# Kernel tuning notes

Hardware: AMD Instinct MI355X
Metric: run time of the kernel (lower is better)

## Reference

```python
import jax, jax.numpy as jnp
import numpy as np
import math

BLOCK = 8
N_COEFF = BLOCK * BLOCK  # 64
N_SAMPLE = 250
SEED = 0  # args.seed

# zigzag order: flat index m*8+n from the hardcoded loc table
ZIGZAG = jnp.array([
    0, 1, 8, 16, 9, 2, 3, 10, 17, 24, 32, 25, 18, 11, 4, 5,
    12, 19, 26, 33, 40, 48, 41, 34, 27, 20, 13, 6, 7, 14, 21, 28,
    35, 42, 49, 56, 57, 50, 43, 36, 29, 22, 15, 23, 30, 37, 44, 51,
    58, 59, 52, 45, 38, 31, 39, 46, 53, 60, 61, 54, 47, 55, 62, 63
], dtype=jnp.int32)


def dct_matrix():
    Q = np.zeros((BLOCK, BLOCK), dtype=np.float32)
    Q[0, :] = math.sqrt(1.0 / BLOCK)
    for i in range(1, BLOCK):
        for j in range(BLOCK):
            Q[i, j] = math.sqrt(2.0 / BLOCK) * math.cos((2 * j + 1) * math.pi * i / (2.0 * BLOCK))
    return jnp.asarray(Q)


def setup_inputs() -> dict:
    key = jax.random.key(0)
    x = jax.random.uniform(key, (64, 3, 512, 512), dtype=jnp.float32)
    return {"x": x}


def reference(x):
    Q = dct_matrix()
    # rgb -> ycbcr, luminance channel only (module discards Cb/Cr)
    x255 = x * 255.0
    y = (0.299 * x255[:, 0] + 0.587 * x255[:, 1] + 0.114 * x255[:, 2]) / 255.0  # [B,H,W]
    B, H, W = y.shape
    a, b = H // BLOCK, W // BLOCK
    # split into 8x8 blocks: [B, a, b, 8, 8]
    blocks = y.reshape(B, a, BLOCK, b, BLOCK).transpose(0, 1, 3, 2, 4)
    # per-block 2D DCT: Q @ block @ Q^T, batched as one einsum
    dct = jnp.einsum('ij,nabjk,lk->nabil', Q, blocks, Q)  # [B,a,b,8,8]
    image_dct_result = dct.transpose(0, 1, 3, 2, 4).reshape(B, 1, H, W)
    # zigzag gather over flattened block coefficients -> [B, 64, a*b]
    dist = dct.reshape(B, a * b, N_COEFF)[:, :, ZIGZAG].transpose(0, 2, 1)
    # per (sample, coefficient) random permutation sampling of 250 blocks
    keys = jax.random.split(jax.random.key(SEED), B * N_COEFF)
    idx = jax.vmap(lambda k: jax.random.permutation(k, a * b)[:N_SAMPLE])(keys)
    idx = idx.reshape(B, N_COEFF, N_SAMPLE)
    dct_coeff_sample = jnp.take_along_axis(dist, idx, axis=2)  # [B,64,250]
    return image_dct_result, dct_coeff_sample
```

## Files before the change

kernel.cpp:

```cpp
#include <hip/hip_runtime.h>
#include <hip/hip_bf16.h>
#include <cstdint>


#define BATCH 64
#define HW 512
#define NBLK 4096
#define NSAMPLE 250
#define IMG_ELEMS (HW * HW)

#define A0 0.35355339059327373f
#define A1 0.49039264020161522f
#define A2 0.46193976625564337f
#define A3 0.41573480615127262f
#define A4 0.35355339059327379f
#define A5 0.27778511650980111f
#define A6 0.19134171618254492f
#define A7 0.09754516100806412f

__constant__ float Qc[8][8] = {
    { A0,  A0,  A0,  A0,  A0,  A0,  A0,  A0},
    { A1,  A3,  A5,  A7, -A7, -A5, -A3, -A1},
    { A2,  A6, -A6, -A2, -A2, -A6,  A6,  A2},
    { A3, -A7, -A1, -A5,  A5,  A1,  A7, -A3},
    { A4, -A4, -A4,  A4,  A4, -A4, -A4,  A4},
    { A5, -A1,  A7,  A3, -A3, -A7,  A1, -A5},
    { A6, -A2,  A2, -A6, -A6,  A2, -A2,  A6},
    { A7, -A5,  A3, -A1,  A1, -A3,  A5, -A7},
};

__constant__ int ZIGZAG[64] = {
    0, 1, 8, 16, 9, 2, 3, 10, 17, 24, 32, 25, 18, 11, 4, 5,
    12, 19, 26, 33, 40, 48, 41, 34, 27, 20, 13, 6, 7, 14, 21, 28,
    35, 42, 49, 56, 57, 50, 43, 36, 29, 22, 15, 23, 30, 37, 44, 51,
    58, 59, 52, 45, 38, 31, 39, 46, 53, 60, 61, 54, 47, 55, 62, 63
};

__device__ __forceinline__ uint32_t rotl32(uint32_t v, int d) {
    return (v << d) | (v >> (32 - d));
}

__device__ __forceinline__ void tf2x32(uint32_t k0, uint32_t k1,
                                       uint32_t x0, uint32_t x1,
                                       uint32_t& o0, uint32_t& o1) {
    uint32_t ks0 = k0, ks1 = k1, ks2 = k0 ^ k1 ^ 0x1BD11BDAu;
    x0 += ks0; x1 += ks1;
#define TF_R(r) { x0 += x1; x1 = rotl32(x1, r); x1 ^= x0; }
    TF_R(13) TF_R(15) TF_R(26) TF_R(6)
    x0 += ks1; x1 += ks2 + 1u;
    TF_R(17) TF_R(29) TF_R(16) TF_R(24)
    x0 += ks2; x1 += ks0 + 2u;
    TF_R(13) TF_R(15) TF_R(26) TF_R(6)
    x0 += ks0; x1 += ks1 + 3u;
    TF_R(17) TF_R(29) TF_R(16) TF_R(24)
    x0 += ks1; x1 += ks2 + 4u;
    TF_R(13) TF_R(15) TF_R(26) TF_R(6)
    x0 += ks2; x1 += ks0 + 5u;
#undef TF_R
    o0 = x0; o1 = x1;
}

__device__ __forceinline__ void build4096(
    uint32_t s0, uint32_t s1,
    uint32_t* __restrict__ pack32, uint32_t* __restrict__ hist,
    int tid, int w, int lane, uint32_t* __restrict__ wsum) {

    __syncthreads();
    ((uint4*)hist)[tid] = make_uint4(0u, 0u, 0u, 0u);
    ((uint4*)hist)[tid + 512] = make_uint4(0u, 0u, 0u, 0u);
    uint32_t keys[8];
#pragma unroll
    for (int e = 0; e < 8; ++e) {
        uint32_t o0, o1;
        tf2x32(s0, s1, 0u, (uint32_t)(tid + e * 512), o0, o1);
        keys[e] = o0 ^ o1;
    }
    __syncthreads();

    uint32_t ord[8];
#pragma unroll
    for (int e = 0; e < 8; ++e)
        ord[e] = atomicAdd(&hist[keys[e] >> 20], 1u);
    __syncthreads();

    uint4 va = ((const uint4*)hist)[tid * 2];
    uint4 vb = ((const uint4*)hist)[tid * 2 + 1];
    uint32_t ssum = va.x + va.y + va.z + va.w + vb.x + vb.y + vb.z + vb.w;
    uint32_t sc = ssum;
#pragma unroll
    for (int off = 1; off < 64; off <<= 1) {
        uint32_t t = __shfl_up(sc, off);
        if (lane >= off) sc += t;
    }
    if (lane == 63) wsum[w] = sc;
    __syncthreads();
    uint32_t ex = sc - ssum;
    for (int ww = 0; ww < w; ++ww) ex += wsum[ww];
    uint32_t p1 = ex + va.x, p2 = p1 + va.y, p3 = p2 + va.z, p4 = p3 + va.w;
    uint32_t p5 = p4 + vb.x, p6 = p5 + vb.y, p7 = p6 + vb.z, p8 = p7 + vb.w;
    ((uint4*)hist)[tid * 2] = make_uint4(p1, p2, p3, p4);
    ((uint4*)hist)[tid * 2 + 1] = make_uint4(p5, p6, p7, p8);
    __syncthreads();

#pragma unroll
    for (int e = 0; e < 8; ++e) {
        uint32_t bkt = keys[e] >> 20;
        uint32_t start = bkt ? hist[bkt - 1] : 0u;
        pack32[start + ord[e]] =
            ((keys[e] & 0xFFFFFu) << 12) | (uint32_t)(tid + e * 512);
    }
}

__device__ __forceinline__ uint32_t select4096(
    const uint32_t* __restrict__ hist, const uint32_t* __restrict__ pack32,
    uint32_t s) {
    uint32_t lo = 0, hi = 4095;
#pragma unroll
    for (int it = 0; it < 12; ++it) {
        uint32_t mid = (lo + hi) >> 1;
        if (hist[mid] > s) hi = mid; else lo = mid + 1;
    }
    uint32_t b = lo;
    uint32_t start = b ? hist[b - 1] : 0u;
    uint32_t L = hist[b] - start;
    uint32_t c = pack32[start];
    if (L > 1) {
        uint32_t k = s - start;
        for (uint32_t cand = 0; cand < L; ++cand) {
            uint32_t cc = pack32[start + cand];
            uint32_t cnt = 0;
            for (uint32_t o = 0; o < L; ++o)
                cnt += (pack32[start + o] < cc) ? 1u : 0u;
            if (cnt == k) { c = cc; break; }
        }
    }
    return c & 0xFFFu;
}

__global__ __launch_bounds__(512, 8) void fused_kernel(
    const float* __restrict__ x, float* __restrict__ out,
    uint32_t* __restrict__ ws) {
    __shared__ __align__(16) uint8_t smem[33280];
    __shared__ uint32_t wsum[8];

    const int tid = threadIdx.x;
    const int grp = (int)blockIdx.x / 9;
    const int rem = (int)blockIdx.x % 9;

    if (rem == 8) {
        int g = grp * 512 + tid;
        int b = g >> 12;
        int rr = g & 4095;
        int ai = rr >> 6, bi = rr & 63;
        int row0 = ai * 8, col0 = bi * 8;
        size_t ib = (size_t)b * 3 * IMG_ELEMS;
        size_t ob = (size_t)b * IMG_ELEMS;

#pragma unroll 1
        for (int p = 0; p < 4; ++p) {
            float acc[2][8];
#pragma unroll
            for (int j = 0; j < 8; ++j) { acc[0][j] = 0.0f; acc[1][j] = 0.0f; }

#pragma unroll 1
            for (int k = 0; k < 8; ++k) {
                size_t off = ib + (size_t)(row0 + k) * HW + col0;
                float y[8];
                {
                    float4 r0 = *(const float4*)(x + off);
                    float4 g0 = *(const float4*)(x + off + IMG_ELEMS);
                    float4 b0 = *(const float4*)(x + off + 2 * IMG_ELEMS);
                    y[0] = (0.299f * (r0.x * 255.0f) + 0.587f * (g0.x * 255.0f) +
                            0.114f * (b0.x * 255.0f)) / 255.0f;
                    y[1] = (0.299f * (r0.y * 255.0f) + 0.587f * (g0.y * 255.0f) +
                            0.114f * (b0.y * 255.0f)) / 255.0f;
                    y[2] = (0.299f * (r0.z * 255.0f) + 0.587f * (g0.z * 255.0f) +
                            0.114f * (b0.z * 255.0f)) / 255.0f;
                    y[3] = (0.299f * (r0.w * 255.0f) + 0.587f * (g0.w * 255.0f) +
                            0.114f * (b0.w * 255.0f)) / 255.0f;
                }
                {
                    float4 r1 = *(const float4*)(x + off + 4);
                    float4 g1 = *(const float4*)(x + off + IMG_ELEMS + 4);
                    float4 b1 = *(const float4*)(x + off + 2 * IMG_ELEMS + 4);
                    y[4] = (0.299f * (r1.x * 255.0f) + 0.587f * (g1.x * 255.0f) +
                            0.114f * (b1.x * 255.0f)) / 255.0f;
                    y[5] = (0.299f * (r1.y * 255.0f) + 0.587f * (g1.y * 255.0f) +
                            0.114f * (b1.y * 255.0f)) / 255.0f;
                    y[6] = (0.299f * (r1.z * 255.0f) + 0.587f * (g1.z * 255.0f) +
                            0.114f * (b1.z * 255.0f)) / 255.0f;
                    y[7] = (0.299f * (r1.w * 255.0f) + 0.587f * (g1.w * 255.0f) +
                            0.114f * (b1.w * 255.0f)) / 255.0f;
                }
                float q0 = Qc[p * 2][k], q1 = Qc[p * 2 + 1][k];
#pragma unroll
                for (int j = 0; j < 8; ++j) {
                    acc[0][j] += q0 * y[j];
                    acc[1][j] += q1 * y[j];
                }
            }

#pragma unroll
            for (int i2 = 0; i2 < 2; ++i2) {
                float d[8];
#pragma unroll
                for (int j = 0; j < 8; ++j) {
                    float s = 0.0f;
#pragma unroll
                    for (int k = 0; k < 8; ++k) s += acc[i2][k] * Qc[j][k];
                    d[j] = s;
                }
                float4* o = (float4*)(out + ob +
                                      (size_t)(row0 + p * 2 + i2) * HW + col0);
                o[0] = make_float4(d[0], d[1], d[2], d[3]);
                o[1] = make_float4(d[4], d[5], d[6], d[7]);
            }
        }
    } else {
        uint32_t* pack32 = (uint32_t*)smem;
        uint32_t* hist = (uint32_t*)(smem + 16384);
        uint16_t* jsel = (uint16_t*)(smem + 32768);

        const int w = tid >> 6;
        const int lane = tid & 63;
        const int gb = grp * 8 + rem;

        uint32_t k0, k1, n0, n1, sA0, sA1, sB0, sB1;
        tf2x32(0u, 0u, 0u, (uint32_t)gb, k0, k1);
        tf2x32(k0, k1, 0u, 0u, n0, n1);
        tf2x32(k0, k1, 0u, 1u, sA0, sA1);
        tf2x32(n0, n1, 0u, 1u, sB0, sB1);

        build4096(sB0, sB1, pack32, hist, tid, w, lane, wsum);
        __syncthreads();
        if (tid < NSAMPLE)
            jsel[tid] = (uint16_t)select4096(hist, pack32, (uint32_t)tid);

        build4096(sA0, sA1, pack32, hist, tid, w, lane, wsum);
        __syncthreads();

        int b = gb >> 6, c = gb & 63;
        int z = ZIGZAG[c];
        int i0z = z >> 3, j0z = z & 7;
        if (tid < NSAMPLE) {
            uint32_t i = select4096(hist, pack32, (uint32_t)jsel[tid]);
            int ai = (int)i >> 6, bi = (int)i & 63;
            ws[(size_t)gb * 256 + tid] =
                (uint32_t)((size_t)b * IMG_ELEMS +
                           (size_t)(ai * 8 + i0z) * HW + (bi * 8 + j0z));
        }
    }
}

__global__ __launch_bounds__(256) void gather_kernel(
    const float* __restrict__ img, const uint32_t* __restrict__ ws,
    float* __restrict__ out2) {
    const int gb = blockIdx.x;
    const int s = threadIdx.x;
    if (s < NSAMPLE)
        out2[(size_t)gb * NSAMPLE + s] = img[ws[(size_t)gb * 256 + s]];
}

extern "C" void kernel_launch(void* const* d_in, const int* in_sizes, int n_in,
                              void* d_out, int out_size, void* d_ws, size_t ws_size,
                              hipStream_t stream) {
    const float* x = (const float*)d_in[0];
    float* out = (float*)d_out;
    uint32_t* ws = (uint32_t*)d_ws;
    fused_kernel<<<512 * 9, 512, 0, stream>>>(x, out, ws);
    gather_kernel<<<BATCH * 64, 256, 0, stream>>>(
        out, ws, out + (size_t)BATCH * IMG_ELEMS);
}
```

Before: 411.4 us.

## Merge DCT work into every permutation block with LDS-staged luma rows

Each of the 4096 blocks now computes the DCT for one 8-pixel-high image row strip before doing its own permutation-sampling work. This replaces the separate DCT-only blocks that ran alongside the sampling blocks. Luma values are staged in shared memory so that the loads and the row transform are spread across threads. The aim is to balance memory-bound and compute-bound work inside each block and to cut the grid size. The risk is that shared memory is reused for pack32 with no visible barrier after the DCT reads, which could race.

```diff
diff --git a/kernel.cpp b/kernel.cpp
--- a/kernel.cpp
+++ b/kernel.cpp
@@ -144,86 +144,81 @@
     __shared__ uint32_t wsum[8];
 
     const int tid = threadIdx.x;
-    const int grp = (int)blockIdx.x / 9;
-    const int rem = (int)blockIdx.x % 9;
-
-    if (rem == 8) {
-        int g = grp * 512 + tid;
-        int b = g >> 12;
-        int rr = g & 4095;
-        int ai = rr >> 6, bi = rr & 63;
-        int row0 = ai * 8, col0 = bi * 8;
-        size_t ib = (size_t)b * 3 * IMG_ELEMS;
-        size_t ob = (size_t)b * IMG_ELEMS;
-
-#pragma unroll 1
-        for (int p = 0; p < 4; ++p) {
-            float acc[2][8];
-#pragma unroll
-            for (int j = 0; j < 8; ++j) { acc[0][j] = 0.0f; acc[1][j] = 0.0f; }
-
-#pragma unroll 1
+    const int gb = blockIdx.x;
+
+    {
+        float* ylds = (float*)smem;
+        const int b = gb >> 6;
+        const int ai = gb & 63;
+        const int row0 = ai * 8;
+        const int h = tid >> 8;
+        const int t2 = tid & 255;
+        const int colbase = h * 256;
+
+        {
+            const int k = t2 >> 5;
+            const int cg = t2 & 31;
+            size_t off = (size_t)b * 3 * IMG_ELEMS + (size_t)(row0 + k) * HW +
+                         colbase + cg * 8;
+            float4 r0 = *(const float4*)(x + off);
+            float4 r1 = *(const float4*)(x + off + 4);
+            float4 g0 = *(const float4*)(x + off + IMG_ELEMS);
+            float4 g1 = *(const float4*)(x + off + IMG_ELEMS + 4);
+            float4 b0 = *(const float4*)(x + off + 2 * IMG_ELEMS);
+            float4 b1 = *(const float4*)(x + off + 2 * IMG_ELEMS + 4);
+            float R[8] = {r0.x, r0.y, r0.z, r0.w, r1.x, r1.y, r1.z, r1.w};
+            float G[8] = {g0.x, g0.y, g0.z, g0.w, g1.x, g1.y, g1.z, g1.w};
+            float B[8] = {b0.x, b0.y, b0.z, b0.w, b1.x, b1.y, b1.z, b1.w};
+            float* yh = ylds + h * 2048 + k * 256;
+#pragma unroll
+            for (int jj = 0; jj < 8; ++jj) {
+                float y = (0.299f * (R[jj] * 255.0f) + 0.587f * (G[jj] * 255.0f) +
+                           0.114f * (B[jj] * 255.0f)) / 255.0f;
+                yh[jj * 32 + cg] = y;
+            }
+        }
+        __syncthreads();
+
+        {
+            const int i = t2 >> 5;
+            const int bi = t2 & 31;
+            const float* yh = ylds + h * 2048;
+            float qrow[8];
+#pragma unroll
+            for (int k = 0; k < 8; ++k) qrow[k] = Qc[i][k];
+
+            float acc[8];
+#pragma unroll
+            for (int j = 0; j < 8; ++j) acc[j] = 0.0f;
+#pragma unroll
             for (int k = 0; k < 8; ++k) {
-                size_t off = ib + (size_t)(row0 + k) * HW + col0;
-                float y[8];
-                {
-                    float4 r0 = *(const float4*)(x + off);
-                    float4 g0 = *(const float4*)(x + off + IMG_ELEMS);
-                    float4 b0 = *(const float4*)(x + off + 2 * IMG_ELEMS);
-                    y[0] = (0.299f * (r0.x * 255.0f) + 0.587f * (g0.x * 255.0f) +
-                            0.114f * (b0.x * 255.0f)) / 255.0f;
-                    y[1] = (0.299f * (r0.y * 255.0f) + 0.587f * (g0.y * 255.0f) +
-                            0.114f * (b0.y * 255.0f)) / 255.0f;
-                    y[2] = (0.299f * (r0.z * 255.0f) + 0.587f * (g0.z * 255.0f) +
-                            0.114f * (b0.z * 255.0f)) / 255.0f;
-                    y[3] = (0.299f * (r0.w * 255.0f) + 0.587f * (g0.w * 255.0f) +
-                            0.114f * (b0.w * 255.0f)) / 255.0f;
-                }
-                {
-                    float4 r1 = *(const float4*)(x + off + 4);
-                    float4 g1 = *(const float4*)(x + off + IMG_ELEMS + 4);
-                    float4 b1 = *(const float4*)(x + off + 2 * IMG_ELEMS + 4);
-                    y[4] = (0.299f * (r1.x * 255.0f) + 0.587f * (g1.x * 255.0f) +
-                            0.114f * (b1.x * 255.0f)) / 255.0f;
-                    y[5] = (0.299f * (r1.y * 255.0f) + 0.587f * (g1.y * 255.0f) +
-                            0.114f * (b1.y * 255.0f)) / 255.0f;
-                    y[6] = (0.299f * (r1.z * 255.0f) + 0.587f * (g1.z * 255.0f) +
-                            0.114f * (b1.z * 255.0f)) / 255.0f;
-                    y[7] = (0.299f * (r1.w * 255.0f) + 0.587f * (g1.w * 255.0f) +
-                            0.114f * (b1.w * 255.0f)) / 255.0f;
-                }
-                float q0 = Qc[p * 2][k], q1 = Qc[p * 2 + 1][k];
-#pragma unroll
-                for (int j = 0; j < 8; ++j) {
-                    acc[0][j] += q0 * y[j];
-                    acc[1][j] += q1 * y[j];
-                }
+#pragma unroll
+                for (int j = 0; j < 8; ++j)
+                    acc[j] += qrow[k] * yh[k * 256 + j * 32 + bi];
             }
 
-#pragma unroll
-            for (int i2 = 0; i2 < 2; ++i2) {
-                float d[8];
-#pragma unroll
-                for (int j = 0; j < 8; ++j) {
-                    float s = 0.0f;
-#pragma unroll
-                    for (int k = 0; k < 8; ++k) s += acc[i2][k] * Qc[j][k];
-                    d[j] = s;
-                }
-                float4* o = (float4*)(out + ob +
-                                      (size_t)(row0 + p * 2 + i2) * HW + col0);
-                o[0] = make_float4(d[0], d[1], d[2], d[3]);
-                o[1] = make_float4(d[4], d[5], d[6], d[7]);
+            float d[8];
+#pragma unroll
+            for (int j = 0; j < 8; ++j) {
+                float s = 0.0f;
+#pragma unroll
+                for (int k = 0; k < 8; ++k) s += acc[k] * Qc[j][k];
+                d[j] = s;
             }
-        }
-    } else {
+            float4* o = (float4*)(out + (size_t)b * IMG_ELEMS +
+                                  (size_t)(row0 + i) * HW + colbase + bi * 8);
+            o[0] = make_float4(d[0], d[1], d[2], d[3]);
+            o[1] = make_float4(d[4], d[5], d[6], d[7]);
+        }
+    }
+
+    {
         uint32_t* pack32 = (uint32_t*)smem;
         uint32_t* hist = (uint32_t*)(smem + 16384);
         uint16_t* jsel = (uint16_t*)(smem + 32768);
 
         const int w = tid >> 6;
         const int lane = tid & 63;
-        const int gb = grp * 8 + rem;
 
         uint32_t k0, k1, n0, n1, sA0, sA1, sB0, sB1;
         tf2x32(0u, 0u, 0u, (uint32_t)gb, k0, k1);
@@ -267,7 +262,7 @@
     const float* x = (const float*)d_in[0];
     float* out = (float*)d_out;
     uint32_t* ws = (uint32_t*)d_ws;
-    fused_kernel<<<512 * 9, 512, 0, stream>>>(x, out, ws);
+    fused_kernel<<<NBLK, 512, 0, stream>>>(x, out, ws);
     gather_kernel<<<BATCH * 64, 256, 0, stream>>>(
         out, ws, out + (size_t)BATCH * IMG_ELEMS);
 }
```

Result: faster. 359.7 us (-12.6%).
